# Optimization experiments

Hardware: AMD Instinct MI355X
Metric: run time of the kernel (lower is better)

Reference implementation:

```python
import jax, jax.numpy as jnp
import numpy as np

K = 6  # kernel size for all locally connected layers

def lc2d(x, w, b, stride):
    # x: [B,C,H,W]; w: [O,C,oh,ow,K*K]; b: [O,oh,ow]
    oh, ow = w.shape[2], w.shape[3]
    s = stride
    # unfold: stack the K*K shifted strided views -> [B,C,oh,ow,K*K]
    patches = jnp.stack([x[:, :, i:i + (oh - 1) * s + 1:s, j:j + (ow - 1) * s + 1:s]
                         for i in range(K) for j in range(K)], axis=-1)
    out = jnp.einsum('bchwk,ochwk->bohw', patches, w)
    return out + b[None]

def maxpool2(x):
    # MaxPool2d(2), floor mode: crop odd trailing row/col then 2x2 max
    B, C, H, W = x.shape
    x = x[:, :, : (H // 2) * 2, : (W // 2) * 2]
    return x.reshape(B, C, H // 2, 2, W // 2, 2).max(axis=(3, 5))

def setup_inputs() -> dict:
    key = jax.random.key(0)
    ks = jax.random.split(key, 9)
    f = lambda k, sh: jax.random.normal(k, sh, dtype=jnp.float32) * 0.05
    return {
        'x':  jax.random.normal(ks[0], (16, 3, 218, 178), dtype=jnp.float32),
        'w1': f(ks[1], (8, 3, 213, 173, 36)),  'b1': f(ks[2], (8, 213, 173)),
        'w2': f(ks[3], (16, 8, 51, 41, 36)),   'b2': f(ks[4], (16, 51, 41)),
        'w3': f(ks[5], (32, 16, 16, 12, 36)),  'b3': f(ks[6], (32, 16, 12)),
        'wf': f(ks[7], (10178, 6144)),         'bf': f(ks[8], (10178,)),
    }

def reference(x, w1, b1, w2, b2, w3, b3, wf, bf):
    h = jax.nn.relu(lc2d(x, w1, b1, stride=1))   # [B,8,213,173]
    h = maxpool2(h)                               # [B,8,106,86]
    h = jax.nn.relu(lc2d(h, w2, b2, stride=2))   # [B,16,51,41]
    h = jax.nn.relu(lc2d(h, w3, b3, stride=3))   # [B,32,16,12]
    h = h.reshape(h.shape[0], -1)                 # [B,6144]
    return h @ wf.T + bf                          # [B,10178]
```

## Files before the change

### kernel.cpp

```cpp
#include <hip/hip_runtime.h>

static __device__ __forceinline__ void fma4(float4& a, float s, float4 v) {
  a.x = fmaf(s, v.x, a.x);
  a.y = fmaf(s, v.y, a.y);
  a.z = fmaf(s, v.z, a.z);
  a.w = fmaf(s, v.w, a.w);
}
static __device__ __forceinline__ float4 relu4(float4 a) {
  return make_float4(fmaxf(a.x, 0.f), fmaxf(a.y, 0.f),
                     fmaxf(a.z, 0.f), fmaxf(a.w, 0.f));
}
typedef float f32x4v __attribute__((ext_vector_type(4)));
typedef short bf16x8 __attribute__((ext_vector_type(8)));
static __device__ __forceinline__ unsigned short f2bf(float f) {
  unsigned u = __float_as_uint(f);
  return (unsigned short)((u + 0x7FFFu + ((u >> 16) & 1u)) >> 16);
}

__global__ void k_transpose_bf16(const float* __restrict__ x,
                                 unsigned short* __restrict__ xtb, int chw,
                                 int total) {
  int p = blockIdx.x * blockDim.x + threadIdx.x;
  if (p >= total) return;
  unsigned d[8];
#pragma unroll
  for (int q = 0; q < 8; ++q) {
    unsigned lo = f2bf(x[(size_t)(2 * q) * chw + p]);
    unsigned hi = f2bf(x[(size_t)(2 * q + 1) * chw + p]);
    d[q] = lo | (hi << 16);
  }
  uint4* o4 = reinterpret_cast<uint4*>(xtb + (size_t)p * 16);
  o4[0] = make_uint4(d[0], d[1], d[2], d[3]);
  o4[1] = make_uint4(d[4], d[5], d[6], d[7]);
}

__global__ __launch_bounds__(256, 4) void k_lc1_mfma(
    const unsigned short* __restrict__ xtb, const float* __restrict__ wgt,
    const float* __restrict__ bias, float* __restrict__ out) {
  constexpr int C = 3, IH = 218, IW = 178, OH = 213, OW = 173;
  constexpr int POS = OH * OW;
  constexpr int KP = 136;
  constexpr int CSTR = IH * IW * 16;
  __shared__ unsigned short wl[16 * 8 * KP];

  const int tid = threadIdx.x;
  const int p0 = blockIdx.x * 16;

  for (int i = tid; i < 3456; i += 256) {
    int pos = i / 216;
    int r = i % 216;
    int o = r / 27;
    int rr = r % 27;
    int c = rr / 9;
    int g4 = rr % 9;
    int gpos = p0 + pos;
    if (gpos >= POS) gpos = POS - 1;
    float4 v = *reinterpret_cast<const float4*>(
        wgt + ((size_t)(o * C + c) * POS + gpos) * 36 + g4 * 4);
    int k0 = (g4 < 8) ? (c * 32 + g4 * 4) : (96 + c * 4);
    unsigned short* d = &wl[(pos * 8 + o) * KP + k0];
    d[0] = f2bf(v.x); d[1] = f2bf(v.y); d[2] = f2bf(v.z); d[3] = f2bf(v.w);
  }
  for (int i = tid; i < 3584; i += 256) {
    int row = i / 28;
    int q = i % 28;
    wl[row * KP + 108 + q] = 0;
  }
  __syncthreads();

  const int l = tid & 63;
  const int wid = tid >> 6;
  const int g = l >> 4;
  const int bb = l & 15;
  const int orow = l & 7;

  int base[8];
  int off3[8];
  bool v3[8];
#pragma unroll
  for (int j = 0; j < 8; ++j) {
    int tap = g * 8 + j;
    base[j] = ((tap / 6) * IW + (tap % 6)) * 16;
    int q = g * 8 + j;
    bool v = (q < 12);
    int cc = v ? (q >> 2) : 0;
    int t3 = v ? (32 + (q & 3)) : 32;
    off3[j] = (cc * IH + 5) * IW * 16 + (t3 - 30) * 16;
    v3[j] = v;
  }

  for (int pp = 0; pp < 4; ++pp) {
    int gpos = p0 + wid * 4 + pp;
    bool valid = gpos < POS;
    int cg = valid ? gpos : POS - 1;
    int h = cg / OW, w = cg % OW;
    int posoff = (h * IW + w) * 16 + bb;
    int lpos = wid * 4 + pp;

    f32x4v acc;
#pragma unroll
    for (int j = 0; j < 4; ++j) {
      int o = g * 4 + j;
      acc[j] = (g < 2) ? bias[(size_t)o * POS + cg] : 0.f;
    }

#pragma unroll
    for (int ch = 0; ch < 4; ++ch) {
      bf16x8 a = *reinterpret_cast<const bf16x8*>(
          &wl[(lpos * 8 + orow) * KP + ch * 32 + g * 8]);
      bf16x8 b;
#pragma unroll
      for (int j = 0; j < 8; ++j) {
        unsigned short xv;
        if (ch < 3)
          xv = xtb[posoff + ch * CSTR + base[j]];
        else
          xv = v3[j] ? xtb[posoff + off3[j]] : (unsigned short)0;
        b[j] = (short)xv;
      }
      acc = __builtin_amdgcn_mfma_f32_16x16x32_bf16(a, b, acc, 0, 0, 0);
    }

    if (valid && g < 2) {
#pragma unroll
      for (int j = 0; j < 4; ++j) {
        int o = g * 4 + j;
        out[((size_t)o * POS + cg) * 16 + bb] = fmaxf(acc[j], 0.f);
      }
    }
  }
}

template <int C, int IH, int IW, int OH, int OW, int S, int O_TOT>
__global__ __launch_bounds__(256) void k_lc_lds_part(
    const float* __restrict__ xt, const float* __restrict__ wgt,
    float* __restrict__ part) {
  constexpr int POS = OH * OW;
  constexpr int NT = (POS + 63) / 64;
  constexpr int OGN = O_TOT / 4;
  __shared__ float4 wl[4 * 64 * 9];
  int tile = blockIdx.x % NT;
  int rem = blockIdx.x / NT;
  int ob0 = (rem % OGN) * 4;
  int c = rem / OGN;
  int p0 = tile * 64;
  int PN = (POS - p0) < 64 ? (POS - p0) : 64;
  int lp = threadIdx.x >> 2, bq = threadIdx.x & 3;
  int fp = p0 + lp;
  bool act = lp < PN;
  int h = act ? fp / OW : 0;
  int w = act ? fp % OW : 0;

  const float4* x4 = reinterpret_cast<const float4*>(xt);
  const float4* w4 = reinterpret_cast<const float4*>(wgt);

  for (int i = threadIdx.x; i < 2304; i += 256) {
    int o_l = i / 576;
    int r = i % 576;
    int pos = r / 9;
    int k4 = r % 9;
    if (pos < PN)
      wl[(o_l * 64 + pos) * 9 + k4] =
          w4[((size_t)((ob0 + o_l) * C + c) * POS + p0 + pos) * 9 + k4];
  }
  __syncthreads();
  if (!act) return;

  float4 acc[4];
#pragma unroll
  for (int o = 0; o < 4; ++o) acc[o] = make_float4(0.f, 0.f, 0.f, 0.f);

  const float4* xc = x4 + ((size_t)(c * IH + h * S) * IW + w * S) * 4 + bq;
#pragma unroll
  for (int k4 = 0; k4 < 9; ++k4) {
    float4 xv[4];
#pragma unroll
    for (int r = 0; r < 4; ++r) {
      int k = k4 * 4 + r;
      xv[r] = xc[((k / 6) * IW + (k % 6)) * 4];
    }
#pragma unroll
    for (int o = 0; o < 4; ++o) {
      float4 wv = wl[(o * 64 + lp) * 9 + k4];
      fma4(acc[o], wv.x, xv[0]);
      fma4(acc[o], wv.y, xv[1]);
      fma4(acc[o], wv.z, xv[2]);
      fma4(acc[o], wv.w, xv[3]);
    }
  }
  float4* pp = reinterpret_cast<float4*>(part) + (size_t)c * (O_TOT * POS * 4);
#pragma unroll
  for (int o = 0; o < 4; ++o)
    pp[((size_t)(ob0 + o) * POS + fp) * 4 + bq] = acc[o];
}

template <int CC, bool A3T>
__global__ void k_combine(const float* __restrict__ part,
                          const float* __restrict__ bias,
                          float* __restrict__ out, int n4total) {
  int p = blockIdx.x * blockDim.x + threadIdx.x;
  if (p >= n4total) return;
  const float4* p4 = reinterpret_cast<const float4*>(part);
  float4 acc = make_float4(0.f, 0.f, 0.f, 0.f);
#pragma unroll
  for (int c = 0; c < CC; ++c) {
    float4 v = p4[(size_t)c * n4total + p];
    acc.x += v.x; acc.y += v.y; acc.z += v.z; acc.w += v.w;
  }
  float bv = bias[p >> 2];
  acc = relu4(make_float4(acc.x + bv, acc.y + bv, acc.z + bv, acc.w + bv));
  if (A3T) {
    int k = p >> 2;
    int bq = p & 3;
    out[(size_t)(bq * 4 + 0) * 6144 + k] = acc.x;
    out[(size_t)(bq * 4 + 1) * 6144 + k] = acc.y;
    out[(size_t)(bq * 4 + 2) * 6144 + k] = acc.z;
    out[(size_t)(bq * 4 + 3) * 6144 + k] = acc.w;
  } else {
    reinterpret_cast<float4*>(out)[p] = acc;
  }
}

__global__ void k_pool(const float* __restrict__ in, float* __restrict__ out,
                       int IH, int IW, int PH, int PW, int total) {
  int t = blockIdx.x * blockDim.x + threadIdx.x;
  if (t >= total) return;
  int bq = t & 3;
  int p = t >> 2;
  int w = p % PW; p /= PW;
  int h = p % PH; p /= PH;
  int o = p;
  const float4* in4 = reinterpret_cast<const float4*>(in);
  size_t r0 = ((size_t)(o * IH + 2 * h) * IW + 2 * w) * 4 + bq;
  float4 a = in4[r0];
  float4 b = in4[r0 + 4];
  float4 c = in4[r0 + (size_t)IW * 4];
  float4 d = in4[r0 + (size_t)IW * 4 + 4];
  float4 m;
  m.x = fmaxf(fmaxf(a.x, b.x), fmaxf(c.x, d.x));
  m.y = fmaxf(fmaxf(a.y, b.y), fmaxf(c.y, d.y));
  m.z = fmaxf(fmaxf(a.z, b.z), fmaxf(c.z, d.z));
  m.w = fmaxf(fmaxf(a.w, b.w), fmaxf(c.w, d.w));
  reinterpret_cast<float4*>(out)[((size_t)(o * PH + h) * PW + w) * 4 + bq] = m;
}

constexpr int FC_N = 10178;
constexpr int FC_K = 6144;
constexpr int FC_KC = 2;
constexpr int FC_KLEN = FC_K / FC_KC;

__global__ __launch_bounds__(256) void k_fc(const float* __restrict__ a3t,
                                            const float* __restrict__ wf,
                                            float* __restrict__ fcp) {
  int wv = threadIdx.x >> 6;
  int l = threadIdx.x & 63;
  int n0 = (blockIdx.x * 4 + wv) * 4;
  int kc = blockIdx.y;
  int kbase = kc * FC_KLEN;

  float acc[64];
#pragma unroll
  for (int j = 0; j < 64; ++j) acc[j] = 0.f;

  int n[4];
#pragma unroll
  for (int m = 0; m < 4; ++m) {
    int nn = n0 + m;
    n[m] = nn < FC_N ? nn : FC_N - 1;
  }

  float4 wr[4];
  {
    int k = kbase + 4 * l;
#pragma unroll
    for (int m = 0; m < 4; ++m)
      wr[m] = *reinterpret_cast<const float4*>(wf + (size_t)n[m] * FC_K + k);
  }

  for (int k0 = 0; k0 < FC_KLEN; k0 += 256) {
    int k = kbase + k0 + 4 * l;
    int kp = (k0 + 256 < FC_KLEN) ? (k + 256) : (kbase + 4 * l);
    float4 wrn[4];
#pragma unroll
    for (int m = 0; m < 4; ++m)
      wrn[m] = *reinterpret_cast<const float4*>(wf + (size_t)n[m] * FC_K + kp);

#pragma unroll
    for (int bg = 0; bg < 4; ++bg) {
      float4 xv[4];
#pragma unroll
      for (int r = 0; r < 4; ++r)
        xv[r] = *reinterpret_cast<const float4*>(a3t +
                    (size_t)(bg * 4 + r) * FC_K + k);
#pragma unroll
      for (int r = 0; r < 4; ++r) {
        int b = bg * 4 + r;
#pragma unroll
        for (int m = 0; m < 4; ++m) {
          int j = b * 4 + m;
          acc[j] = fmaf(wr[m].x, xv[r].x, acc[j]);
          acc[j] = fmaf(wr[m].y, xv[r].y, acc[j]);
          acc[j] = fmaf(wr[m].z, xv[r].z, acc[j]);
          acc[j] = fmaf(wr[m].w, xv[r].w, acc[j]);
        }
      }
      __builtin_amdgcn_sched_barrier(0);
    }
#pragma unroll
    for (int m = 0; m < 4; ++m) wr[m] = wrn[m];
  }

#pragma unroll
  for (int s = 0; s < 6; ++s) {
    int mask = 1 << s;
    int bit = (l >> s) & 1;
#pragma unroll
    for (int t = 0; t < 32; ++t) {
      if (t < (64 >> (s + 1))) {
        float e = acc[2 * t] + __shfl_xor(acc[2 * t], mask, 64);
        float o = acc[2 * t + 1] + __shfl_xor(acc[2 * t + 1], mask, 64);
        acc[t] = bit ? o : e;
      }
    }
  }

  int b = l >> 2;
  int m = l & 3;
  int nn = n0 + m;
  if (nn < FC_N)
    fcp[((size_t)kc * 16 + b) * FC_N + nn] = acc[0];
}

__global__ void k_fc_comb(const float* __restrict__ fcp,
                          const float* __restrict__ bf,
                          float* __restrict__ out, int total) {
  int t = blockIdx.x * blockDim.x + threadIdx.x;
  if (t >= total) return;
  unsigned n = (unsigned)t % (unsigned)FC_N;
  float s = bf[n];
#pragma unroll
  for (int kc = 0; kc < FC_KC; ++kc) s += fcp[(size_t)kc * 16 * FC_N + t];
  out[t] = s;
}

static inline int cdiv(int a, int b) { return (a + b - 1) / b; }

extern "C" void kernel_launch(void* const* d_in, const int* in_sizes, int n_in,
                              void* d_out, int out_size, void* d_ws,
                              size_t ws_size, hipStream_t stream) {
  const float* x  = (const float*)d_in[0];
  const float* w1 = (const float*)d_in[1];
  const float* b1 = (const float*)d_in[2];
  const float* w2 = (const float*)d_in[3];
  const float* b2 = (const float*)d_in[4];
  const float* w3 = (const float*)d_in[5];
  const float* b3 = (const float*)d_in[6];
  const float* wf = (const float*)d_in[7];
  const float* bf = (const float*)d_in[8];
  float* out = (float*)d_out;

  float* ws = (float*)d_ws;
  float* xt     = ws;
  float* a1     = ws + 1862592;
  float* a1p    = ws + 6579264;
  float* a2     = ws + 7746112;
  float* a3t    = ws + 8281408;
  unsigned short* xtb = (unsigned short*)xt;
  float* l2part = a1;
  float* l3part = xt;
  float* fcp    = a1p;

  {
    int total = 3 * 218 * 178;
    k_transpose_bf16<<<cdiv(total, 256), 256, 0, stream>>>(x, xtb, total,
                                                           total);
  }
  {
    k_lc1_mfma<<<cdiv(213 * 173, 16), 256, 0, stream>>>(xtb, w1, b1, a1);
  }
  {
    int total = 4 * 8 * 106 * 86;
    k_pool<<<cdiv(total, 256), 256, 0, stream>>>(a1, a1p, 213, 173, 106, 86,
                                                 total);
  }
  {
    k_lc_lds_part<8, 106, 86, 51, 41, 2, 16>
        <<<33 * 4 * 8, 256, 0, stream>>>(a1p, w2, l2part);
  }
  {
    int n4 = 16 * 2091 * 4;
    k_combine<8, false><<<cdiv(n4, 256), 256, 0, stream>>>(l2part, b2, a2, n4);
  }
  {
    k_lc_lds_part<16, 51, 41, 16, 12, 3, 32>
        <<<3 * 8 * 16, 256, 0, stream>>>(a2, w3, l3part);
  }
  {
    int n4 = 32 * 192 * 4;
    k_combine<16, true><<<cdiv(n4, 256), 256, 0, stream>>>(l3part, b3, a3t, n4);
  }
  {
    dim3 grid(cdiv(FC_N, 16), FC_KC);
    k_fc<<<grid, 256, 0, stream>>>(a3t, wf, fcp);
  }
  {
    int total = 16 * FC_N;
    k_fc_comb<<<cdiv(total, 256), 256, 0, stream>>>(fcp, bf, out, total);
  }
}
```

Before: 194.5 us.

## Fuse channel reduction into LC2/LC3 kernels, drop combine passes, nontemporal FC weights

Replaces the split-channel partial-sum kernels and their separate combine kernels for layers 2 and 3 with one kernel that loops over input channels internally, adding bias and ReLU in-register before writing the final activation. This removes the partial-sum round trips through global memory and two kernel launches. The cost is far fewer blocks (264 and 96 instead of 1056 and 384) plus a per-channel LDS reload with two barriers per channel, which may leave the GPU underoccupied. It also switches the FC weight loads to nontemporal loads and repacks the bf16 gather in layer 1 into 32-bit words.

```diff
diff --git a/kernel.cpp b/kernel.cpp
--- a/kernel.cpp
+++ b/kernel.cpp
@@ -9,6 +9,11 @@
 static __device__ __forceinline__ float4 relu4(float4 a) {
   return make_float4(fmaxf(a.x, 0.f), fmaxf(a.y, 0.f),
                      fmaxf(a.z, 0.f), fmaxf(a.w, 0.f));
+}
+typedef float floatv4 __attribute__((ext_vector_type(4)));
+static __device__ __forceinline__ float4 ntld4(const float* p) {
+  floatv4 v = __builtin_nontemporal_load(reinterpret_cast<const floatv4*>(p));
+  return make_float4(v.x, v.y, v.z, v.w);
 }
 typedef float f32x4v __attribute__((ext_vector_type(4)));
 typedef short bf16x8 __attribute__((ext_vector_type(8)));
@@ -108,17 +113,24 @@
     for (int ch = 0; ch < 4; ++ch) {
       bf16x8 a = *reinterpret_cast<const bf16x8*>(
           &wl[(lpos * 8 + orow) * KP + ch * 32 + g * 8]);
-      bf16x8 b;
-#pragma unroll
-      for (int j = 0; j < 8; ++j) {
-        unsigned short xv;
-        if (ch < 3)
-          xv = xtb[posoff + ch * CSTR + base[j]];
-        else
-          xv = v3[j] ? xtb[posoff + off3[j]] : (unsigned short)0;
-        b[j] = (short)xv;
-      }
-      acc = __builtin_amdgcn_mfma_f32_16x16x32_bf16(a, b, acc, 0, 0, 0);
+      unsigned short t[8];
+      if (ch < 3) {
+        const unsigned short* xp = xtb + posoff + ch * CSTR;
+#pragma unroll
+        for (int j = 0; j < 8; ++j) t[j] = xp[base[j]];
+      } else {
+#pragma unroll
+        for (int j = 0; j < 8; ++j)
+          t[j] = v3[j] ? xtb[posoff + off3[j]] : (unsigned short)0;
+      }
+      union {
+        unsigned u[4];
+        bf16x8 v;
+      } B;
+#pragma unroll
+      for (int q = 0; q < 4; ++q)
+        B.u[q] = (unsigned)t[2 * q] | ((unsigned)t[2 * q + 1] << 16);
+      acc = __builtin_amdgcn_mfma_f32_16x16x32_bf16(a, B.v, acc, 0, 0, 0);
     }
 
     if (valid && g < 2) {
@@ -131,18 +143,16 @@
   }
 }
 
-template <int C, int IH, int IW, int OH, int OW, int S, int O_TOT>
-__global__ __launch_bounds__(256) void k_lc_lds_part(
+template <int C, int IH, int IW, int OH, int OW, int S, int O_BLK, bool A3T>
+__global__ __launch_bounds__(256) void k_lc_full(
     const float* __restrict__ xt, const float* __restrict__ wgt,
-    float* __restrict__ part) {
+    const float* __restrict__ bias, float* __restrict__ out) {
   constexpr int POS = OH * OW;
   constexpr int NT = (POS + 63) / 64;
-  constexpr int OGN = O_TOT / 4;
-  __shared__ float4 wl[4 * 64 * 9];
+  constexpr int SN = O_BLK * 576;
+  __shared__ float4 wl[O_BLK * 64 * 9];
   int tile = blockIdx.x % NT;
-  int rem = blockIdx.x / NT;
-  int ob0 = (rem % OGN) * 4;
-  int c = rem / OGN;
+  int ob0 = (blockIdx.x / NT) * O_BLK;
   int p0 = tile * 64;
   int PN = (POS - p0) < 64 ? (POS - p0) : 64;
   int lp = threadIdx.x >> 2, bq = threadIdx.x & 3;
@@ -151,73 +161,64 @@
   int h = act ? fp / OW : 0;
   int w = act ? fp % OW : 0;
 
+  float4 acc[O_BLK];
+#pragma unroll
+  for (int o = 0; o < O_BLK; ++o) {
+    float bv = act ? bias[(size_t)(ob0 + o) * POS + fp] : 0.f;
+    acc[o] = make_float4(bv, bv, bv, bv);
+  }
+
   const float4* x4 = reinterpret_cast<const float4*>(xt);
   const float4* w4 = reinterpret_cast<const float4*>(wgt);
 
-  for (int i = threadIdx.x; i < 2304; i += 256) {
-    int o_l = i / 576;
-    int r = i % 576;
-    int pos = r / 9;
-    int k4 = r % 9;
-    if (pos < PN)
-      wl[(o_l * 64 + pos) * 9 + k4] =
-          w4[((size_t)((ob0 + o_l) * C + c) * POS + p0 + pos) * 9 + k4];
-  }
-  __syncthreads();
-  if (!act) return;
-
-  float4 acc[4];
-#pragma unroll
-  for (int o = 0; o < 4; ++o) acc[o] = make_float4(0.f, 0.f, 0.f, 0.f);
-
-  const float4* xc = x4 + ((size_t)(c * IH + h * S) * IW + w * S) * 4 + bq;
-#pragma unroll
-  for (int k4 = 0; k4 < 9; ++k4) {
-    float4 xv[4];
-#pragma unroll
-    for (int r = 0; r < 4; ++r) {
-      int k = k4 * 4 + r;
-      xv[r] = xc[((k / 6) * IW + (k % 6)) * 4];
-    }
-#pragma unroll
-    for (int o = 0; o < 4; ++o) {
-      float4 wv = wl[(o * 64 + lp) * 9 + k4];
-      fma4(acc[o], wv.x, xv[0]);
-      fma4(acc[o], wv.y, xv[1]);
-      fma4(acc[o], wv.z, xv[2]);
-      fma4(acc[o], wv.w, xv[3]);
-    }
-  }
-  float4* pp = reinterpret_cast<float4*>(part) + (size_t)c * (O_TOT * POS * 4);
-#pragma unroll
-  for (int o = 0; o < 4; ++o)
-    pp[((size_t)(ob0 + o) * POS + fp) * 4 + bq] = acc[o];
-}
-
-template <int CC, bool A3T>
-__global__ void k_combine(const float* __restrict__ part,
-                          const float* __restrict__ bias,
-                          float* __restrict__ out, int n4total) {
-  int p = blockIdx.x * blockDim.x + threadIdx.x;
-  if (p >= n4total) return;
-  const float4* p4 = reinterpret_cast<const float4*>(part);
-  float4 acc = make_float4(0.f, 0.f, 0.f, 0.f);
-#pragma unroll
-  for (int c = 0; c < CC; ++c) {
-    float4 v = p4[(size_t)c * n4total + p];
-    acc.x += v.x; acc.y += v.y; acc.z += v.z; acc.w += v.w;
-  }
-  float bv = bias[p >> 2];
-  acc = relu4(make_float4(acc.x + bv, acc.y + bv, acc.z + bv, acc.w + bv));
-  if (A3T) {
-    int k = p >> 2;
-    int bq = p & 3;
-    out[(size_t)(bq * 4 + 0) * 6144 + k] = acc.x;
-    out[(size_t)(bq * 4 + 1) * 6144 + k] = acc.y;
-    out[(size_t)(bq * 4 + 2) * 6144 + k] = acc.z;
-    out[(size_t)(bq * 4 + 3) * 6144 + k] = acc.w;
-  } else {
-    reinterpret_cast<float4*>(out)[p] = acc;
+  for (int c = 0; c < C; ++c) {
+    __syncthreads();
+    for (int i = threadIdx.x; i < SN; i += 256) {
+      int o_l = i / 576;
+      int r = i % 576;
+      int pos = r / 9;
+      int k4 = r % 9;
+      if (pos < PN)
+        wl[(o_l * 64 + pos) * 9 + k4] =
+            w4[((size_t)((ob0 + o_l) * C + c) * POS + p0 + pos) * 9 + k4];
+    }
+    __syncthreads();
+    if (act) {
+      const float4* xc = x4 + ((size_t)(c * IH + h * S) * IW + w * S) * 4 + bq;
+#pragma unroll
+      for (int k4 = 0; k4 < 9; ++k4) {
+        float4 xv[4];
+#pragma unroll
+        for (int r = 0; r < 4; ++r) {
+          int k = k4 * 4 + r;
+          xv[r] = xc[((k / 6) * IW + (k % 6)) * 4];
+        }
+#pragma unroll
+        for (int o = 0; o < O_BLK; ++o) {
+          float4 wv = wl[(o * 64 + lp) * 9 + k4];
+          fma4(acc[o], wv.x, xv[0]);
+          fma4(acc[o], wv.y, xv[1]);
+          fma4(acc[o], wv.z, xv[2]);
+          fma4(acc[o], wv.w, xv[3]);
+        }
+      }
+    }
+  }
+  if (act) {
+#pragma unroll
+    for (int o = 0; o < O_BLK; ++o) {
+      float4 r = relu4(acc[o]);
+      if (A3T) {
+        int k = (ob0 + o) * POS + fp;
+        out[(size_t)(bq * 4 + 0) * 6144 + k] = r.x;
+        out[(size_t)(bq * 4 + 1) * 6144 + k] = r.y;
+        out[(size_t)(bq * 4 + 2) * 6144 + k] = r.z;
+        out[(size_t)(bq * 4 + 3) * 6144 + k] = r.w;
+      } else {
+        reinterpret_cast<float4*>(out)[((size_t)(ob0 + o) * POS + fp) * 4 + bq] =
+            r;
+      }
+    }
   }
 }
 
@@ -273,8 +274,7 @@
   {
     int k = kbase + 4 * l;
 #pragma unroll
-    for (int m = 0; m < 4; ++m)
-      wr[m] = *reinterpret_cast<const float4*>(wf + (size_t)n[m] * FC_K + k);
+    for (int m = 0; m < 4; ++m) wr[m] = ntld4(wf + (size_t)n[m] * FC_K + k);
   }
 
   for (int k0 = 0; k0 < FC_KLEN; k0 += 256) {
@@ -282,8 +282,7 @@
     int kp = (k0 + 256 < FC_KLEN) ? (k + 256) : (kbase + 4 * l);
     float4 wrn[4];
 #pragma unroll
-    for (int m = 0; m < 4; ++m)
-      wrn[m] = *reinterpret_cast<const float4*>(wf + (size_t)n[m] * FC_K + kp);
+    for (int m = 0; m < 4; ++m) wrn[m] = ntld4(wf + (size_t)n[m] * FC_K + kp);
 
 #pragma unroll
     for (int bg = 0; bg < 4; ++bg) {
@@ -360,15 +359,13 @@
   float* out = (float*)d_out;
 
   float* ws = (float*)d_ws;
-  float* xt     = ws;
-  float* a1     = ws + 1862592;
-  float* a1p    = ws + 6579264;
-  float* a2     = ws + 7746112;
-  float* a3t    = ws + 8281408;
+  float* xt   = ws;
+  float* a1   = ws + 1862592;
+  float* a1p  = ws + 6579264;
+  float* a2   = ws + 7746112;
+  float* a3t  = ws + 8281408;
   unsigned short* xtb = (unsigned short*)xt;
-  float* l2part = a1;
-  float* l3part = xt;
-  float* fcp    = a1p;
+  float* fcp  = a1p;
 
   {
     int total = 3 * 218 * 178;
@@ -384,20 +381,12 @@
                                                  total);
   }
   {
-    k_lc_lds_part<8, 106, 86, 51, 41, 2, 16>
-        <<<33 * 4 * 8, 256, 0, stream>>>(a1p, w2, l2part);
-  }
-  {
-    int n4 = 16 * 2091 * 4;
-    k_combine<8, false><<<cdiv(n4, 256), 256, 0, stream>>>(l2part, b2, a2, n4);
-  }
-  {
-    k_lc_lds_part<16, 51, 41, 16, 12, 3, 32>
-        <<<3 * 8 * 16, 256, 0, stream>>>(a2, w3, l3part);
-  }
-  {
-    int n4 = 32 * 192 * 4;
-    k_combine<16, true><<<cdiv(n4, 256), 256, 0, stream>>>(l3part, b3, a3t, n4);
+    k_lc_full<8, 106, 86, 51, 41, 2, 2, false>
+        <<<33 * 8, 256, 0, stream>>>(a1p, w2, b2, a2);
+  }
+  {
+    k_lc_full<16, 51, 41, 16, 12, 3, 1, true>
+        <<<3 * 32, 256, 0, stream>>>(a2, w3, b3, a3t);
   }
   {
     dim3 grid(cdiv(FC_N, 16), FC_KC);
```

New measurement: 226.4 us. 1.16x slower.
